# Kernel tuning notes

Measured on AMD Instinct MI355X. Metric: run time of the kernel, lower is better.

Reference implementation:

```python
import jax, jax.numpy as jnp
import numpy as np

N = 8192
H = 1024
E = 8
K = 2

def setup_inputs() -> dict:
    key = jax.random.key(0)
    ks = jax.random.split(key, 8)
    x = jax.random.normal(ks[0], (N, H), dtype=jnp.float32)
    grad = jax.random.normal(ks[1], (N, 1), dtype=jnp.float32)
    s_r = 1.0 / np.sqrt(H + 1)
    s1 = 1.0 / np.sqrt(H)
    s2 = 1.0 / np.sqrt(4 * H)
    Wr = jax.random.normal(ks[2], (H + 1, E), dtype=jnp.float32) * s_r
    br = jnp.zeros((E,), dtype=jnp.float32)
    W1 = jax.random.normal(ks[3], (E, H, 4 * H), dtype=jnp.float32) * s1
    b1 = jnp.zeros((E, 4 * H), dtype=jnp.float32)
    W2 = jax.random.normal(ks[4], (E, 4 * H, H), dtype=jnp.float32) * s2
    b2 = jnp.zeros((E, H), dtype=jnp.float32)
    return {"x": x, "grad": grad, "Wr": Wr, "br": br, "W1": W1, "b1": b1, "W2": W2, "b2": b2}

def reference(x, grad, Wr, br, W1, b1, W2, b2):
    # router on [x, grad]
    router_in = jnp.concatenate([x, grad], axis=-1)            # [N, H+1]
    logits = router_in @ Wr + br                               # [N, E]
    probs = jax.nn.softmax(logits, axis=-1)
    topk_probs, topk_idx = jax.lax.top_k(probs, K)             # [N, K]
    # combine weight per (token, expert): sum over k of prob * onehot(idx)
    onehot = jax.nn.one_hot(topk_idx, E, dtype=x.dtype)        # [N, K, E]
    cw = jnp.einsum('nk,nke->ne', topk_probs, onehot)          # [N, E]
    # dense all-expert MLP (equivalent math to masked dispatch/scatter-add)
    h = jnp.einsum('nh,ehf->enf', x, W1) + b1[:, None, :]      # [E, N, 4H]
    h = jax.nn.gelu(h, approximate=False)                      # torch nn.GELU = exact erf
    o = jnp.einsum('enf,efh->enh', h, W2) + b2[:, None, :]     # [E, N, H]
    out = jnp.einsum('enh,ne->nh', o, cw)                      # [N, H]
    return out
```

## Files before the change

kernel.cpp:

```cpp
#include <hip/hip_runtime.h>
#include <hip/hip_bf16.h>
#include <stdint.h>


#define NTOK 8192
#define HD   1024
#define NE   8
#define FF   4096
#define MAXT 136

typedef float  f32x4 __attribute__((ext_vector_type(4)));
typedef _Float16 half8 __attribute__((ext_vector_type(8)));
typedef _Float16 half4 __attribute__((ext_vector_type(4)));

#define AS1 __attribute__((address_space(1)))
#define AS3 __attribute__((address_space(3)))

__device__ __forceinline__ void gload16(const void* g, void* l) {
  __builtin_amdgcn_global_load_lds((AS1 void*)g, (AS3 void*)l, 16, 0, 0);
}

__device__ __forceinline__ bool tile_lookup(const int* __restrict__ counts,
                                            int t, int& e, int& m0, int& cnt) {
#pragma unroll
  for (int i = 0; i < NE; ++i) {
    int c = counts[i];
    int nt = (c + 127) >> 7;
    if (t < nt) { e = i; m0 = t << 7; cnt = c; return true; }
    t -= nt;
  }
  return false;
}

__global__ __launch_bounds__(256) void convx_k(const float* __restrict__ x,
                                               _Float16* __restrict__ xh) {
  int i = blockIdx.x * 256 + threadIdx.x;
  float4 v = ((const float4*)x)[i];
  half4 h = {(_Float16)v.x, (_Float16)v.y, (_Float16)v.z, (_Float16)v.w};
  ((half4*)xh)[i] = h;
}

__global__ __launch_bounds__(256) void transc_k(const float* __restrict__ src,
                                                _Float16* __restrict__ dst,
                                                int R, int C) {
  __shared__ float t[64][65];
  const int e = blockIdx.z;
  const size_t eb = (size_t)e * R * C;
  const int r0 = blockIdx.y * 64, c0 = blockIdx.x * 64;
  const int tid = threadIdx.x;
#pragma unroll
  for (int i = 0; i < 4; ++i) {
    int idx = tid + i * 256;
    int r = idx >> 4, c = (idx & 15) * 4;
    float4 v = *(const float4*)(src + eb + (size_t)(r0 + r) * C + (c0 + c));
    t[r][c] = v.x; t[r][c + 1] = v.y; t[r][c + 2] = v.z; t[r][c + 3] = v.w;
  }
  __syncthreads();
#pragma unroll
  for (int i = 0; i < 4; ++i) {
    int idx = tid + i * 256;
    int cr = idx >> 4, r4 = (idx & 15) * 4;
    half4 o = {(_Float16)t[r4][cr], (_Float16)t[r4 + 1][cr],
               (_Float16)t[r4 + 2][cr], (_Float16)t[r4 + 3][cr]};
    *(half4*)(dst + eb + (size_t)(c0 + cr) * R + (r0 + r4)) = o;
  }
}

__global__ __launch_bounds__(256) void router_k(const float* __restrict__ x,
                                                const float* __restrict__ grad,
                                                const float* __restrict__ Wr,
                                                const float* __restrict__ br,
                                                int* __restrict__ counts,
                                                int* __restrict__ tokL,
                                                float* __restrict__ wL) {
  const int lane = threadIdx.x & 63;
  const int n = blockIdx.x * 4 + (threadIdx.x >> 6);
  float acc[8] = {0.f, 0.f, 0.f, 0.f, 0.f, 0.f, 0.f, 0.f};
  const float* xr = x + (size_t)n * HD;
#pragma unroll 4
  for (int i = 0; i < 16; ++i) {
    float xv = xr[i * 64 + lane];
    const float* wr = Wr + (size_t)(i * 64 + lane) * NE;
    float4 w0 = *(const float4*)wr;
    float4 w1 = *(const float4*)(wr + 4);
    acc[0] += xv * w0.x; acc[1] += xv * w0.y; acc[2] += xv * w0.z; acc[3] += xv * w0.w;
    acc[4] += xv * w1.x; acc[5] += xv * w1.y; acc[6] += xv * w1.z; acc[7] += xv * w1.w;
  }
#pragma unroll
  for (int off = 32; off > 0; off >>= 1)
#pragma unroll
    for (int e = 0; e < 8; ++e) acc[e] += __shfl_xor(acc[e], off, 64);
  if (lane == 0) {
    float gv = grad[n];
    float lg[8];
#pragma unroll
    for (int e = 0; e < 8; ++e) lg[e] = acc[e] + gv * Wr[HD * NE + e] + br[e];
    float m = lg[0];
#pragma unroll
    for (int e = 1; e < 8; ++e) m = fmaxf(m, lg[e]);
    float s = 0.f, p[8];
#pragma unroll
    for (int e = 0; e < 8; ++e) { p[e] = expf(lg[e] - m); s += p[e]; }
    int i1 = 0;
#pragma unroll
    for (int e = 1; e < 8; ++e) if (lg[e] > lg[i1]) i1 = e;
    int i2 = (i1 == 0) ? 1 : 0;
#pragma unroll
    for (int e = 0; e < 8; ++e) if (e != i1 && lg[e] > lg[i2]) i2 = e;
    float inv = 1.0f / s;
    int p1 = atomicAdd(&counts[i1], 1);
    tokL[i1 * NTOK + p1] = n; wL[i1 * NTOK + p1] = p[i1] * inv;
    int p2 = atomicAdd(&counts[i2], 1);
    tokL[i2 * NTOK + p2] = n; wL[i2 * NTOK + p2] = p[i2] * inv;
  }
}

__global__ void prefix_k(const int* __restrict__ counts, int* __restrict__ base) {
  if (threadIdx.x == 0) {
    int s = 0;
    for (int e = 0; e < NE; ++e) { base[e] = s; s += counts[e]; }
  }
}

__global__ __launch_bounds__(256) void gemm1_k(const _Float16* __restrict__ xh,
                                               const _Float16* __restrict__ w1t,
                                               const float* __restrict__ b1,
                                               const int* __restrict__ tokL,
                                               const int* __restrict__ counts,
                                               const int* __restrict__ base,
                                               _Float16* __restrict__ hbuf) {
  int e, m0, cnt;
  if (!tile_lookup(counts, blockIdx.y, e, m0, cnt)) return;
  const int n0 = blockIdx.x * 128;
  const int hb = base[e];

  __shared__ __align__(16) char smem[65536];

  const int tid = threadIdx.x;
  const int lane = tid & 63;
  const int wid = tid >> 6;
  const int wm = wid >> 1, wn = wid & 1;
  const int lr = lane & 15, lk = lane >> 4;

  const int srow = tid >> 3;
  const int kk = ((tid & 7) ^ (srow & 7)) << 3;
  const _Float16* aSrc[4];
  const _Float16* bSrc[4];
#pragma unroll
  for (int c = 0; c < 4; ++c) {
    int r = srow + 32 * c;
    int gm = m0 + r; if (gm >= cnt) gm = cnt - 1;
    int t = tokL[e * NTOK + gm];
    aSrc[c] = xh + (size_t)t * HD + kk;
    bSrc[c] = w1t + ((size_t)e * FF + n0 + r) * HD + kk;
  }
  const int ldsOff = (tid & 192) * 16;

  f32x4 acc[4][4] = {};

  auto stage = [&](int p) {
    char* A = smem + p * 32768 + ldsOff;
    char* B = smem + p * 32768 + 16384 + ldsOff;
#pragma unroll
    for (int c = 0; c < 4; ++c) {
      gload16(aSrc[c], A + c * 4096);
      gload16(bSrc[c], B + c * 4096);
      aSrc[c] += 64; bSrc[c] += 64;
    }
  };
  auto compute = [&](int p) {
    const char* A = smem + p * 32768;
    const char* B = A + 16384;
#pragma unroll
    for (int k2 = 0; k2 < 2; ++k2) {
      half8 a[4], b[4];
#pragma unroll
      for (int mf = 0; mf < 4; ++mf) {
        int row = wm * 64 + mf * 16 + lr;
        int off = row * 128 + (((k2 * 64) + (lk << 4)) ^ ((row & 7) << 4));
        a[mf] = *(const half8*)(A + off);
      }
#pragma unroll
      for (int nf = 0; nf < 4; ++nf) {
        int row = wn * 64 + nf * 16 + lr;
        int off = row * 128 + (((k2 * 64) + (lk << 4)) ^ ((row & 7) << 4));
        b[nf] = *(const half8*)(B + off);
      }
#pragma unroll
      for (int mf = 0; mf < 4; ++mf)
#pragma unroll
        for (int nf = 0; nf < 4; ++nf)
          acc[mf][nf] = __builtin_amdgcn_mfma_f32_16x16x32_f16(a[mf], b[nf], acc[mf][nf], 0, 0, 0);
    }
  };

  stage(0);
  asm volatile("s_waitcnt vmcnt(0)" ::: "memory");
  __builtin_amdgcn_s_barrier();
  const int NK = HD / 64;
  for (int kt = 0; kt < NK - 1; ++kt) {
    int p = kt & 1;
    stage(p ^ 1);
    compute(p);
    asm volatile("s_waitcnt lgkmcnt(0)" ::: "memory");
    asm volatile("s_waitcnt vmcnt(0)" ::: "memory");
    __builtin_amdgcn_s_barrier();
  }
  compute((NK - 1) & 1);
  asm volatile("s_waitcnt lgkmcnt(0)" ::: "memory");
  __builtin_amdgcn_s_barrier();

#define OSTR 132
  _Float16* ot = (_Float16*)smem;
#pragma unroll
  for (int nf = 0; nf < 4; ++nf) {
    int col = wn * 64 + nf * 16 + lr;
    float bias = b1[(size_t)e * FF + n0 + col];
#pragma unroll
    for (int mf = 0; mf < 4; ++mf) {
      int rb = wm * 64 + mf * 16 + lk * 4;
#pragma unroll
      for (int j = 0; j < 4; ++j) {
        float v = acc[mf][nf][j] + bias;
        v = 0.5f * v * (1.0f + erff(v * 0.70710678118654752f));
        ot[(rb + j) * OSTR + col] = (_Float16)v;
      }
    }
  }
  asm volatile("s_waitcnt lgkmcnt(0)" ::: "memory");
  __builtin_amdgcn_s_barrier();
#pragma unroll
  for (int i = 0; i < 8; ++i) {
    int row = i * 16 + (tid >> 4);
    int gm = m0 + row;
    half8 v = *(const half8*)(ot + row * OSTR + (tid & 15) * 8);
    if (gm < cnt)
      *(half8*)(hbuf + (size_t)(hb + gm) * FF + n0 + (tid & 15) * 8) = v;
  }
#undef OSTR
}

__global__ __launch_bounds__(256) void gemm2_k(const _Float16* __restrict__ hbuf,
                                               const _Float16* __restrict__ w2t,
                                               const float* __restrict__ b2,
                                               const int* __restrict__ tokL,
                                               const float* __restrict__ wL,
                                               const int* __restrict__ counts,
                                               const int* __restrict__ base,
                                               float* __restrict__ out) {
  int e, m0, cnt;
  if (!tile_lookup(counts, blockIdx.y, e, m0, cnt)) return;
  const int n0 = blockIdx.x * 128;
  const int hb = base[e];

  __shared__ __align__(16) char smem[65536];

  const int tid = threadIdx.x;
  const int lane = tid & 63;
  const int wid = tid >> 6;
  const int wm = wid >> 1, wn = wid & 1;
  const int lr = lane & 15, lk = lane >> 4;

  const int srow = tid >> 3;
  const int kk = ((tid & 7) ^ (srow & 7)) << 3;
  const _Float16* aSrc[4];
  const _Float16* bSrc[4];
#pragma unroll
  for (int c = 0; c < 4; ++c) {
    int r = srow + 32 * c;
    int gm = m0 + r; if (gm >= cnt) gm = cnt - 1;
    aSrc[c] = hbuf + (size_t)(hb + gm) * FF + kk;
    bSrc[c] = w2t + ((size_t)e * HD + n0 + r) * FF + kk;
  }
  const int ldsOff = (tid & 192) * 16;

  f32x4 acc[4][4] = {};

  auto stage = [&](int p) {
    char* A = smem + p * 32768 + ldsOff;
    char* B = smem + p * 32768 + 16384 + ldsOff;
#pragma unroll
    for (int c = 0; c < 4; ++c) {
      gload16(aSrc[c], A + c * 4096);
      gload16(bSrc[c], B + c * 4096);
      aSrc[c] += 64; bSrc[c] += 64;
    }
  };
  auto compute = [&](int p) {
    const char* A = smem + p * 32768;
    const char* B = A + 16384;
#pragma unroll
    for (int k2 = 0; k2 < 2; ++k2) {
      half8 a[4], b[4];
#pragma unroll
      for (int mf = 0; mf < 4; ++mf) {
        int row = wm * 64 + mf * 16 + lr;
        int off = row * 128 + (((k2 * 64) + (lk << 4)) ^ ((row & 7) << 4));
        a[mf] = *(const half8*)(A + off);
      }
#pragma unroll
      for (int nf = 0; nf < 4; ++nf) {
        int row = wn * 64 + nf * 16 + lr;
        int off = row * 128 + (((k2 * 64) + (lk << 4)) ^ ((row & 7) << 4));
        b[nf] = *(const half8*)(B + off);
      }
#pragma unroll
      for (int mf = 0; mf < 4; ++mf)
#pragma unroll
        for (int nf = 0; nf < 4; ++nf)
          acc[mf][nf] = __builtin_amdgcn_mfma_f32_16x16x32_f16(a[mf], b[nf], acc[mf][nf], 0, 0, 0);
    }
  };

  stage(0);
  asm volatile("s_waitcnt vmcnt(0)" ::: "memory");
  __builtin_amdgcn_s_barrier();
  const int NK = FF / 64;
  for (int kt = 0; kt < NK - 1; ++kt) {
    int p = kt & 1;
    stage(p ^ 1);
    compute(p);
    asm volatile("s_waitcnt lgkmcnt(0)" ::: "memory");
    asm volatile("s_waitcnt vmcnt(0)" ::: "memory");
    __builtin_amdgcn_s_barrier();
  }
  compute((NK - 1) & 1);

#pragma unroll
  for (int mf = 0; mf < 4; ++mf) {
    int mb = wm * 64 + mf * 16 + lk * 4;
    int tk[4]; float pw[4]; bool val[4];
#pragma unroll
    for (int j = 0; j < 4; ++j) {
      int gm = m0 + mb + j;
      val[j] = (gm < cnt);
      int idx = e * NTOK + (val[j] ? gm : 0);
      tk[j] = tokL[idx];
      pw[j] = wL[idx];
    }
#pragma unroll
    for (int nf = 0; nf < 4; ++nf) {
      int n = n0 + wn * 64 + nf * 16 + lr;
      float b2v = b2[(size_t)e * HD + n];
#pragma unroll
      for (int j = 0; j < 4; ++j) {
        if (val[j]) {
          atomicAdd(out + (size_t)tk[j] * HD + n, pw[j] * (acc[mf][nf][j] + b2v));
        }
      }
    }
  }
}

extern "C" void kernel_launch(void* const* d_in, const int* in_sizes, int n_in,
                              void* d_out, int out_size, void* d_ws, size_t ws_size,
                              hipStream_t stream) {
  const float* x    = (const float*)d_in[0];
  const float* grad = (const float*)d_in[1];
  const float* Wr   = (const float*)d_in[2];
  const float* br   = (const float*)d_in[3];
  const float* W1   = (const float*)d_in[4];
  const float* b1   = (const float*)d_in[5];
  const float* W2   = (const float*)d_in[6];
  const float* b2   = (const float*)d_in[7];
  float* out = (float*)d_out;

  char* ws = (char*)d_ws;
  int*      counts = (int*)(ws + 0);
  int*      basep  = (int*)(ws + 128);
  int*      tokL   = (int*)(ws + 256);
  float*    wL     = (float*)(ws + 262400);
  _Float16* xh     = (_Float16*)(ws + 524544);
  _Float16* w1t    = (_Float16*)(ws + 17301760);
  _Float16* w2t    = (_Float16*)(ws + 84410624);
  _Float16* hbuf   = (_Float16*)(ws + 151519488);
  if (ws_size < 285737216ull) return;

  hipMemsetAsync(counts, 0, 64, stream);
  hipMemsetAsync(out, 0, (size_t)NTOK * HD * 4, stream);

  convx_k<<<(NTOK * HD / 4) / 256, 256, 0, stream>>>(x, xh);
  transc_k<<<dim3(FF / 64, HD / 64, NE), 256, 0, stream>>>(W1, w1t, HD, FF);
  transc_k<<<dim3(HD / 64, FF / 64, NE), 256, 0, stream>>>(W2, w2t, FF, HD);
  router_k<<<NTOK / 4, 256, 0, stream>>>(x, grad, Wr, br, counts, tokL, wL);
  prefix_k<<<1, 64, 0, stream>>>(counts, basep);

  gemm1_k<<<dim3(FF / 128, MAXT), 256, 0, stream>>>(xh, w1t, b1, tokL, counts, basep, hbuf);
  gemm2_k<<<dim3(HD / 128, MAXT), 256, 0, stream>>>(hbuf, w2t, b2, tokL, wL, counts, basep, out);
}
```

Baseline: 1.057 ms.

## Use 256x256 8-wave GEMM tiles with phased pipeline, split-K gemm2, fuse x conversion

Both expert GEMMs move from 128x128 tiles with 4 waves to 256x256 tiles with 8 waves. They use a 4-quadrant ping-pong schedule that interleaves LDS reads, async global-to-LDS loads and MFMA bursts, with s_setprio and finer vmcnt waits. gemm2 is split over K into two halves via blockIdx.z to keep the grid large, and only the first split adds the bias. The fp16 conversion of x is folded into the router kernel, so the separate conversion kernel is gone. The larger tiles raise reuse and reduce launch tiles, but padding waste on partial expert tiles grows and the split doubles the atomic traffic into the output.

```diff
diff --git a/kernel.cpp b/kernel.cpp
--- a/kernel.cpp
+++ b/kernel.cpp
@@ -7,7 +7,7 @@
 #define HD   1024
 #define NE   8
 #define FF   4096
-#define MAXT 136
+#define MAXT 72
 
 typedef float  f32x4 __attribute__((ext_vector_type(4)));
 typedef _Float16 half8 __attribute__((ext_vector_type(8)));
@@ -25,19 +25,11 @@
 #pragma unroll
   for (int i = 0; i < NE; ++i) {
     int c = counts[i];
-    int nt = (c + 127) >> 7;
-    if (t < nt) { e = i; m0 = t << 7; cnt = c; return true; }
+    int nt = (c + 255) >> 8;
+    if (t < nt) { e = i; m0 = t << 8; cnt = c; return true; }
     t -= nt;
   }
   return false;
-}
-
-__global__ __launch_bounds__(256) void convx_k(const float* __restrict__ x,
-                                               _Float16* __restrict__ xh) {
-  int i = blockIdx.x * 256 + threadIdx.x;
-  float4 v = ((const float4*)x)[i];
-  half4 h = {(_Float16)v.x, (_Float16)v.y, (_Float16)v.z, (_Float16)v.w};
-  ((half4*)xh)[i] = h;
 }
 
 __global__ __launch_bounds__(256) void transc_k(const float* __restrict__ src,
@@ -72,14 +64,17 @@
                                                 const float* __restrict__ br,
                                                 int* __restrict__ counts,
                                                 int* __restrict__ tokL,
-                                                float* __restrict__ wL) {
+                                                float* __restrict__ wL,
+                                                _Float16* __restrict__ xh) {
   const int lane = threadIdx.x & 63;
   const int n = blockIdx.x * 4 + (threadIdx.x >> 6);
   float acc[8] = {0.f, 0.f, 0.f, 0.f, 0.f, 0.f, 0.f, 0.f};
   const float* xr = x + (size_t)n * HD;
+  _Float16* xo = xh + (size_t)n * HD;
 #pragma unroll 4
   for (int i = 0; i < 16; ++i) {
     float xv = xr[i * 64 + lane];
+    xo[i * 64 + lane] = (_Float16)xv;
     const float* wr = Wr + (size_t)(i * 64 + lane) * NE;
     float4 w0 = *(const float4*)wr;
     float4 w1 = *(const float4*)(wr + 4);
@@ -122,231 +117,243 @@
   }
 }
 
-__global__ __launch_bounds__(256) void gemm1_k(const _Float16* __restrict__ xh,
-                                               const _Float16* __restrict__ w1t,
-                                               const float* __restrict__ b1,
-                                               const int* __restrict__ tokL,
-                                               const int* __restrict__ counts,
-                                               const int* __restrict__ base,
-                                               _Float16* __restrict__ hbuf) {
+
+#define DSA(BUF, MH)                                                          \
+  {                                                                           \
+    const char* _ab = smem + (BUF)*65536 + (MH)*16384;                        \
+    _Pragma("unroll") for (int mf = 0; mf < 4; ++mf) {                        \
+      int row = wm * 64 + mf * 16 + lr;                                       \
+      _Pragma("unroll") for (int k2 = 0; k2 < 2; ++k2) {                      \
+        int off = row * 128 + ((k2 * 64 + (lk << 4)) ^ ((row & 7) << 4));     \
+        af[mf][k2] = *(const half8*)(_ab + off);                              \
+      }                                                                       \
+    }                                                                         \
+  }
+
+#define DSB(BUF, NH)                                                          \
+  {                                                                           \
+    const char* _bb = smem + (BUF)*65536 + 32768 + (NH)*16384;                \
+    _Pragma("unroll") for (int nf = 0; nf < 2; ++nf) {                        \
+      int row = wn * 32 + nf * 16 + lr;                                       \
+      _Pragma("unroll") for (int k2 = 0; k2 < 2; ++k2) {                      \
+        int off = row * 128 + ((k2 * 64 + (lk << 4)) ^ ((row & 7) << 4));     \
+        bf[nf][k2] = *(const half8*)(_bb + off);                              \
+      }                                                                       \
+    }                                                                         \
+  }
+
+#define MFMAQ(MH, NH)                                                         \
+  __builtin_amdgcn_s_setprio(1);                                              \
+  _Pragma("unroll") for (int mf = 0; mf < 4; ++mf)                            \
+  _Pragma("unroll") for (int nf = 0; nf < 2; ++nf)                            \
+  _Pragma("unroll") for (int k2 = 0; k2 < 2; ++k2)                            \
+    acc[(MH)*4 + mf][(NH)*2 + nf] = __builtin_amdgcn_mfma_f32_16x16x32_f16(   \
+        af[mf][k2], bf[nf][k2], acc[(MH)*4 + mf][(NH)*2 + nf], 0, 0, 0);      \
+  __builtin_amdgcn_s_setprio(0);
+
+#define PH(BUF, MH, NH, STG, VM)                                              \
+  do {                                                                        \
+    DSA(BUF, MH); DSB(BUF, NH);                                               \
+    STG;                                                                      \
+    if (VM) asm volatile("s_waitcnt vmcnt(4)" ::: "memory");                  \
+    __builtin_amdgcn_s_barrier();                                             \
+    asm volatile("s_waitcnt lgkmcnt(0)" ::: "memory");                        \
+    MFMAQ(MH, NH);                                                            \
+    __builtin_amdgcn_s_barrier();                                             \
+  } while (0)
+
+#define STAGE_A(BUF, H, KIDX)                                                 \
+  {                                                                           \
+    char* _d = smem + (BUF)*65536 + (H)*16384 + (wid << 10);                  \
+    gload16(aP[(H)*2 + 0] + (KIDX)*64, _d);                                   \
+    gload16(aP[(H)*2 + 1] + (KIDX)*64, _d + 8192);                            \
+  }
+#define STAGE_B(BUF, H, KIDX, LDB)                                            \
+  {                                                                           \
+    char* _d = smem + (BUF)*65536 + 32768 + (H)*16384 + (wid << 10);          \
+    gload16(bP + (size_t)((H)*128) * (LDB) + (KIDX)*64, _d);                  \
+    gload16(bP + (size_t)((H)*128 + 64) * (LDB) + (KIDX)*64, _d + 8192);      \
+  }
+
+__global__ __launch_bounds__(512, 2) void gemm1_k(const _Float16* __restrict__ xh,
+                                                  const _Float16* __restrict__ w1t,
+                                                  const float* __restrict__ b1,
+                                                  const int* __restrict__ tokL,
+                                                  const int* __restrict__ counts,
+                                                  const int* __restrict__ base,
+                                                  _Float16* __restrict__ hbuf) {
   int e, m0, cnt;
   if (!tile_lookup(counts, blockIdx.y, e, m0, cnt)) return;
-  const int n0 = blockIdx.x * 128;
+  const int n0 = blockIdx.x * 256;
   const int hb = base[e];
 
-  __shared__ __align__(16) char smem[65536];
+  __shared__ __align__(16) char smem[131072];
 
   const int tid = threadIdx.x;
   const int lane = tid & 63;
   const int wid = tid >> 6;
-  const int wm = wid >> 1, wn = wid & 1;
+  const int wm = wid & 1, wn = wid >> 1;
   const int lr = lane & 15, lk = lane >> 4;
 
   const int srow = tid >> 3;
   const int kk = ((tid & 7) ^ (srow & 7)) << 3;
-  const _Float16* aSrc[4];
-  const _Float16* bSrc[4];
-#pragma unroll
-  for (int c = 0; c < 4; ++c) {
-    int r = srow + 32 * c;
-    int gm = m0 + r; if (gm >= cnt) gm = cnt - 1;
-    int t = tokL[e * NTOK + gm];
-    aSrc[c] = xh + (size_t)t * HD + kk;
-    bSrc[c] = w1t + ((size_t)e * FF + n0 + r) * HD + kk;
-  }
-  const int ldsOff = (tid & 192) * 16;
-
-  f32x4 acc[4][4] = {};
-
-  auto stage = [&](int p) {
-    char* A = smem + p * 32768 + ldsOff;
-    char* B = smem + p * 32768 + 16384 + ldsOff;
-#pragma unroll
-    for (int c = 0; c < 4; ++c) {
-      gload16(aSrc[c], A + c * 4096);
-      gload16(bSrc[c], B + c * 4096);
-      aSrc[c] += 64; bSrc[c] += 64;
-    }
-  };
-  auto compute = [&](int p) {
-    const char* A = smem + p * 32768;
-    const char* B = A + 16384;
-#pragma unroll
-    for (int k2 = 0; k2 < 2; ++k2) {
-      half8 a[4], b[4];
-#pragma unroll
-      for (int mf = 0; mf < 4; ++mf) {
-        int row = wm * 64 + mf * 16 + lr;
-        int off = row * 128 + (((k2 * 64) + (lk << 4)) ^ ((row & 7) << 4));
-        a[mf] = *(const half8*)(A + off);
+  const _Float16* aP[4];
+#pragma unroll
+  for (int h = 0; h < 2; ++h)
+#pragma unroll
+    for (int j = 0; j < 2; ++j) {
+      int r = h * 128 + j * 64 + srow;
+      int gm = m0 + r; if (gm >= cnt) gm = cnt - 1;
+      aP[h * 2 + j] = xh + (size_t)tokL[e * NTOK + gm] * HD + kk;
+    }
+  const _Float16* bP = w1t + ((size_t)e * FF + n0 + srow) * HD + kk;
+
+  f32x4 acc[8][4] = {};
+  half8 af[4][2], bf[2][2];
+
+  STAGE_A(0, 0, 0); STAGE_A(0, 1, 0); STAGE_B(0, 0, 0, HD); STAGE_B(0, 1, 0, HD);
+  STAGE_A(1, 0, 1); STAGE_B(1, 1, 1, HD);
+  asm volatile("s_waitcnt vmcnt(4)" ::: "memory");
+  __builtin_amdgcn_s_barrier();
+
+  const int NK = HD / 64;
+  for (int it = 0; it < NK / 2; ++it) {
+    int t1 = 2 * it + 1;
+    int t0n = 2 * it + 2; if (t0n > NK - 1) t0n = NK - 1;
+    int t1n = 2 * it + 3; if (t1n > NK - 1) t1n = NK - 1;
+    PH(0, 0, 0, STAGE_A(1, 1, t1), 0);
+    PH(0, 0, 1, STAGE_B(1, 0, t1, HD), 0);
+    PH(0, 1, 1, STAGE_A(0, 0, t0n), 0);
+    PH(0, 1, 0, STAGE_B(0, 1, t0n, HD), 1);
+    PH(1, 0, 0, STAGE_A(0, 1, t0n), 0);
+    PH(1, 0, 1, STAGE_B(0, 0, t0n, HD), 0);
+    PH(1, 1, 1, STAGE_A(1, 0, t1n), 0);
+    PH(1, 1, 0, STAGE_B(1, 1, t1n, HD), 1);
+  }
+  asm volatile("s_waitcnt vmcnt(0) lgkmcnt(0)" ::: "memory");
+  __builtin_amdgcn_s_barrier();
+
+#pragma unroll
+  for (int ni = 0; ni < 4; ++ni) {
+    const int nh = ni >> 1, nf = ni & 1;
+    int col = nh * 128 + wn * 32 + nf * 16 + lr;
+    float bias = b1[(size_t)e * FF + n0 + col];
+#pragma unroll
+    for (int mi = 0; mi < 8; ++mi) {
+      const int mh = mi >> 2, mf = mi & 3;
+      int rb = mh * 128 + wm * 64 + mf * 16 + lk * 4;
+#pragma unroll
+      for (int j = 0; j < 4; ++j) {
+        float v = acc[mi][ni][j] + bias;
+        v = 0.5f * v * (1.0f + erff(v * 0.70710678118654752f));
+        int row = rb + j;
+        *(_Float16*)(smem + row * 512 + ((col * 2) ^ ((row & 7) << 4))) = (_Float16)v;
       }
-#pragma unroll
-      for (int nf = 0; nf < 4; ++nf) {
-        int row = wn * 64 + nf * 16 + lr;
-        int off = row * 128 + (((k2 * 64) + (lk << 4)) ^ ((row & 7) << 4));
-        b[nf] = *(const half8*)(B + off);
-      }
-#pragma unroll
-      for (int mf = 0; mf < 4; ++mf)
-#pragma unroll
-        for (int nf = 0; nf < 4; ++nf)
-          acc[mf][nf] = __builtin_amdgcn_mfma_f32_16x16x32_f16(a[mf], b[nf], acc[mf][nf], 0, 0, 0);
-    }
-  };
-
-  stage(0);
-  asm volatile("s_waitcnt vmcnt(0)" ::: "memory");
-  __builtin_amdgcn_s_barrier();
-  const int NK = HD / 64;
-  for (int kt = 0; kt < NK - 1; ++kt) {
-    int p = kt & 1;
-    stage(p ^ 1);
-    compute(p);
-    asm volatile("s_waitcnt lgkmcnt(0)" ::: "memory");
-    asm volatile("s_waitcnt vmcnt(0)" ::: "memory");
-    __builtin_amdgcn_s_barrier();
-  }
-  compute((NK - 1) & 1);
+    }
+  }
   asm volatile("s_waitcnt lgkmcnt(0)" ::: "memory");
   __builtin_amdgcn_s_barrier();
-
-#define OSTR 132
-  _Float16* ot = (_Float16*)smem;
-#pragma unroll
-  for (int nf = 0; nf < 4; ++nf) {
-    int col = wn * 64 + nf * 16 + lr;
-    float bias = b1[(size_t)e * FF + n0 + col];
-#pragma unroll
-    for (int mf = 0; mf < 4; ++mf) {
-      int rb = wm * 64 + mf * 16 + lk * 4;
-#pragma unroll
-      for (int j = 0; j < 4; ++j) {
-        float v = acc[mf][nf][j] + bias;
-        v = 0.5f * v * (1.0f + erff(v * 0.70710678118654752f));
-        ot[(rb + j) * OSTR + col] = (_Float16)v;
-      }
-    }
-  }
-  asm volatile("s_waitcnt lgkmcnt(0)" ::: "memory");
-  __builtin_amdgcn_s_barrier();
-#pragma unroll
-  for (int i = 0; i < 8; ++i) {
-    int row = i * 16 + (tid >> 4);
+#pragma unroll
+  for (int ps = 0; ps < 16; ++ps) {
+    int row = ps * 16 + (tid >> 5);
+    int c = tid & 31;
+    int lc = c ^ (row & 7);
+    half8 v = *(const half8*)(smem + row * 512 + c * 16);
     int gm = m0 + row;
-    half8 v = *(const half8*)(ot + row * OSTR + (tid & 15) * 8);
     if (gm < cnt)
-      *(half8*)(hbuf + (size_t)(hb + gm) * FF + n0 + (tid & 15) * 8) = v;
-  }
-#undef OSTR
-}
-
-__global__ __launch_bounds__(256) void gemm2_k(const _Float16* __restrict__ hbuf,
-                                               const _Float16* __restrict__ w2t,
-                                               const float* __restrict__ b2,
-                                               const int* __restrict__ tokL,
-                                               const float* __restrict__ wL,
-                                               const int* __restrict__ counts,
-                                               const int* __restrict__ base,
-                                               float* __restrict__ out) {
+      *(half8*)(hbuf + (size_t)(hb + gm) * FF + n0 + lc * 8) = v;
+  }
+}
+
+__global__ __launch_bounds__(512, 2) void gemm2_k(const _Float16* __restrict__ hbuf,
+                                                  const _Float16* __restrict__ w2t,
+                                                  const float* __restrict__ b2,
+                                                  const int* __restrict__ tokL,
+                                                  const float* __restrict__ wL,
+                                                  const int* __restrict__ counts,
+                                                  const int* __restrict__ base,
+                                                  float* __restrict__ out) {
   int e, m0, cnt;
   if (!tile_lookup(counts, blockIdx.y, e, m0, cnt)) return;
-  const int n0 = blockIdx.x * 128;
+  const int n0 = blockIdx.x * 256;
+  const int ks = blockIdx.z;
   const int hb = base[e];
 
-  __shared__ __align__(16) char smem[65536];
+  __shared__ __align__(16) char smem[131072];
 
   const int tid = threadIdx.x;
   const int lane = tid & 63;
   const int wid = tid >> 6;
-  const int wm = wid >> 1, wn = wid & 1;
+  const int wm = wid & 1, wn = wid >> 1;
   const int lr = lane & 15, lk = lane >> 4;
 
   const int srow = tid >> 3;
   const int kk = ((tid & 7) ^ (srow & 7)) << 3;
-  const _Float16* aSrc[4];
-  const _Float16* bSrc[4];
-#pragma unroll
-  for (int c = 0; c < 4; ++c) {
-    int r = srow + 32 * c;
-    int gm = m0 + r; if (gm >= cnt) gm = cnt - 1;
-    aSrc[c] = hbuf + (size_t)(hb + gm) * FF + kk;
-    bSrc[c] = w2t + ((size_t)e * HD + n0 + r) * FF + kk;
-  }
-  const int ldsOff = (tid & 192) * 16;
-
-  f32x4 acc[4][4] = {};
-
-  auto stage = [&](int p) {
-    char* A = smem + p * 32768 + ldsOff;
-    char* B = smem + p * 32768 + 16384 + ldsOff;
-#pragma unroll
-    for (int c = 0; c < 4; ++c) {
-      gload16(aSrc[c], A + c * 4096);
-      gload16(bSrc[c], B + c * 4096);
-      aSrc[c] += 64; bSrc[c] += 64;
-    }
-  };
-  auto compute = [&](int p) {
-    const char* A = smem + p * 32768;
-    const char* B = A + 16384;
-#pragma unroll
-    for (int k2 = 0; k2 < 2; ++k2) {
-      half8 a[4], b[4];
-#pragma unroll
-      for (int mf = 0; mf < 4; ++mf) {
-        int row = wm * 64 + mf * 16 + lr;
-        int off = row * 128 + (((k2 * 64) + (lk << 4)) ^ ((row & 7) << 4));
-        a[mf] = *(const half8*)(A + off);
-      }
-#pragma unroll
-      for (int nf = 0; nf < 4; ++nf) {
-        int row = wn * 64 + nf * 16 + lr;
-        int off = row * 128 + (((k2 * 64) + (lk << 4)) ^ ((row & 7) << 4));
-        b[nf] = *(const half8*)(B + off);
-      }
-#pragma unroll
-      for (int mf = 0; mf < 4; ++mf)
-#pragma unroll
-        for (int nf = 0; nf < 4; ++nf)
-          acc[mf][nf] = __builtin_amdgcn_mfma_f32_16x16x32_f16(a[mf], b[nf], acc[mf][nf], 0, 0, 0);
-    }
-  };
-
-  stage(0);
-  asm volatile("s_waitcnt vmcnt(0)" ::: "memory");
-  __builtin_amdgcn_s_barrier();
-  const int NK = FF / 64;
-  for (int kt = 0; kt < NK - 1; ++kt) {
-    int p = kt & 1;
-    stage(p ^ 1);
-    compute(p);
-    asm volatile("s_waitcnt lgkmcnt(0)" ::: "memory");
-    asm volatile("s_waitcnt vmcnt(0)" ::: "memory");
-    __builtin_amdgcn_s_barrier();
-  }
-  compute((NK - 1) & 1);
-
-#pragma unroll
-  for (int mf = 0; mf < 4; ++mf) {
-    int mb = wm * 64 + mf * 16 + lk * 4;
-    int tk[4]; float pw[4]; bool val[4];
+  const size_t kbase = (size_t)ks * 2048;
+  const _Float16* aP[4];
+#pragma unroll
+  for (int h = 0; h < 2; ++h)
+#pragma unroll
+    for (int j = 0; j < 2; ++j) {
+      int r = h * 128 + j * 64 + srow;
+      int gm = m0 + r; if (gm >= cnt) gm = cnt - 1;
+      aP[h * 2 + j] = hbuf + (size_t)(hb + gm) * FF + kbase + kk;
+    }
+  const _Float16* bP = w2t + ((size_t)e * HD + n0 + srow) * FF + kbase + kk;
+
+  f32x4 acc[8][4] = {};
+  half8 af[4][2], bf[2][2];
+
+  STAGE_A(0, 0, 0); STAGE_A(0, 1, 0); STAGE_B(0, 0, 0, FF); STAGE_B(0, 1, 0, FF);
+  STAGE_A(1, 0, 1); STAGE_B(1, 1, 1, FF);
+  asm volatile("s_waitcnt vmcnt(4)" ::: "memory");
+  __builtin_amdgcn_s_barrier();
+
+  const int NK = 2048 / 64;
+  for (int it = 0; it < NK / 2; ++it) {
+    int t1 = 2 * it + 1;
+    int t0n = 2 * it + 2; if (t0n > NK - 1) t0n = NK - 1;
+    int t1n = 2 * it + 3; if (t1n > NK - 1) t1n = NK - 1;
+    PH(0, 0, 0, STAGE_A(1, 1, t1), 0);
+    PH(0, 0, 1, STAGE_B(1, 0, t1, FF), 0);
+    PH(0, 1, 1, STAGE_A(0, 0, t0n), 0);
+    PH(0, 1, 0, STAGE_B(0, 1, t0n, FF), 1);
+    PH(1, 0, 0, STAGE_A(0, 1, t0n), 0);
+    PH(1, 0, 1, STAGE_B(0, 0, t0n, FF), 0);
+    PH(1, 1, 1, STAGE_A(1, 0, t1n), 0);
+    PH(1, 1, 0, STAGE_B(1, 1, t1n, FF), 1);
+  }
+  asm volatile("s_waitcnt vmcnt(0) lgkmcnt(0)" ::: "memory");
+  __builtin_amdgcn_s_barrier();
+
+  float b2v[4];
+#pragma unroll
+  for (int ni = 0; ni < 4; ++ni) {
+    const int nh = ni >> 1, nf = ni & 1;
+    int n = n0 + nh * 128 + wn * 32 + nf * 16 + lr;
+    b2v[ni] = (ks == 0) ? b2[(size_t)e * HD + n] : 0.0f;
+  }
+#pragma unroll
+  for (int mi = 0; mi < 8; ++mi) {
+    const int mh = mi >> 2, mf = mi & 3;
+    int rb = m0 + mh * 128 + wm * 64 + mf * 16 + lk * 4;
+    int tk[4]; float pw[4]; bool ok[4];
 #pragma unroll
     for (int j = 0; j < 4; ++j) {
-      int gm = m0 + mb + j;
-      val[j] = (gm < cnt);
-      int idx = e * NTOK + (val[j] ? gm : 0);
+      int gm = rb + j;
+      ok[j] = (gm < cnt);
+      int idx = e * NTOK + (ok[j] ? gm : 0);
       tk[j] = tokL[idx];
       pw[j] = wL[idx];
     }
 #pragma unroll
-    for (int nf = 0; nf < 4; ++nf) {
-      int n = n0 + wn * 64 + nf * 16 + lr;
-      float b2v = b2[(size_t)e * HD + n];
+    for (int ni = 0; ni < 4; ++ni) {
+      const int nh = ni >> 1, nf = ni & 1;
+      int n = n0 + nh * 128 + wn * 32 + nf * 16 + lr;
 #pragma unroll
       for (int j = 0; j < 4; ++j) {
-        if (val[j]) {
-          atomicAdd(out + (size_t)tk[j] * HD + n, pw[j] * (acc[mf][nf][j] + b2v));
-        }
+        if (ok[j])
+          atomicAdd(out + (size_t)tk[j] * HD + n, pw[j] * (acc[mi][ni][j] + b2v[ni]));
       }
     }
   }
@@ -379,12 +386,11 @@
   hipMemsetAsync(counts, 0, 64, stream);
   hipMemsetAsync(out, 0, (size_t)NTOK * HD * 4, stream);
 
-  convx_k<<<(NTOK * HD / 4) / 256, 256, 0, stream>>>(x, xh);
   transc_k<<<dim3(FF / 64, HD / 64, NE), 256, 0, stream>>>(W1, w1t, HD, FF);
   transc_k<<<dim3(HD / 64, FF / 64, NE), 256, 0, stream>>>(W2, w2t, FF, HD);
-  router_k<<<NTOK / 4, 256, 0, stream>>>(x, grad, Wr, br, counts, tokL, wL);
+  router_k<<<NTOK / 4, 256, 0, stream>>>(x, grad, Wr, br, counts, tokL, wL, xh);
   prefix_k<<<1, 64, 0, stream>>>(counts, basep);
 
-  gemm1_k<<<dim3(FF / 128, MAXT), 256, 0, stream>>>(xh, w1t, b1, tokL, counts, basep, hbuf);
-  gemm2_k<<<dim3(HD / 128, MAXT), 256, 0, stream>>>(hbuf, w2t, b2, tokL, wL, counts, basep, out);
-}
+  gemm1_k<<<dim3(FF / 256, MAXT), 512, 0, stream>>>(xh, w1t, b1, tokL, counts, basep, hbuf);
+  gemm2_k<<<dim3(HD / 256, MAXT, 2), 512, 0, stream>>>(hbuf, w2t, b2, tokL, wL, counts, basep, out);
+}
```

Result: no change. 1.055 ms (-0.2%).
